# Optimization experiments

Measured on AMD Instinct MI355X. Metric: run time of the kernel, lower is better.

The kernel has to match this reference:

```python
import jax, jax.numpy as jnp
import numpy as np

# ---- dims ----
B0, CIN, Hh, Ww = 8, 256, 96, 96
SPLIT = 8
DM = CIN // SPLIT            # 32  per-split d_model
EXPAND = 2
DIN = EXPAND * DM            # 64  d_inner
DSTATE = 64
DCONV = 3
HEADDIM = 8
NH = DIN // HEADDIM          # 8 heads
DOUT = 256
CHUNK = 32
D_IN_PROJ = 2 * DIN + 2 * DSTATE + NH  # 264
CONV_CH = DIN + 2 * DSTATE   # 192


def setup_inputs() -> dict:
    key = jax.random.key(0)
    ks = jax.random.split(key, 10)
    x = jax.random.normal(ks[0], (B0, CIN, Hh, Ww), jnp.float32)
    inp = {
        'x': x,
        'ln_w': jnp.ones((CIN,), jnp.float32),
        'ln_b': jnp.zeros((CIN,), jnp.float32),
        'skip_scale': jnp.ones((1,), jnp.float32),
        'proj_w': jax.random.normal(ks[1], (CIN, DOUT), jnp.float32) / np.sqrt(CIN),
        'proj_b': jnp.zeros((DOUT,), jnp.float32),
        'W_in': jax.random.normal(ks[2], (DM, D_IN_PROJ), jnp.float32) / np.sqrt(DM),
        'conv_w': jax.random.normal(ks[3], (CONV_CH, 1, DCONV), jnp.float32) * 0.3,
        'conv_b': jnp.zeros((CONV_CH,), jnp.float32),
        'dt_bias': jax.random.normal(ks[4], (NH,), jnp.float32) * 0.5,
        'A_log': jnp.log(jnp.arange(1.0, NH + 1.0, dtype=jnp.float32)),
        'D': jax.random.normal(ks[5], (NH,), jnp.float32) * 0.5,
        'rms_w': jnp.ones((DIN,), jnp.float32),
        'W_out': jax.random.normal(ks[6], (DIN, DM), jnp.float32) / np.sqrt(DIN),
    }
    return inp


def _layernorm(x, w, b, eps=1e-5):
    mu = jnp.mean(x, -1, keepdims=True)
    xc = x - mu
    var = jnp.mean(xc * xc, -1, keepdims=True)
    return xc * jax.lax.rsqrt(var + eps) * w + b


def _ssd(x, A, Bm, Cm, chunk):
    # x: (b,l,h,p)  A: (b,l,h)  Bm/Cm: (b,l,n); chunked SSD (Mamba2 minimal)
    b, l, h, p = x.shape
    n = Bm.shape[-1]
    nc = l // chunk
    xc = x.reshape(b, nc, chunk, h, p)
    Ac = A.reshape(b, nc, chunk, h).transpose(0, 3, 1, 2)  # (b,h,c,l)
    Bc = Bm.reshape(b, nc, chunk, n)
    Cc = Cm.reshape(b, nc, chunk, n)
    ac = jnp.cumsum(Ac, -1)                                 # (b,h,c,l)
    seg = ac[..., :, None] - ac[..., None, :]
    mask = jnp.tril(jnp.ones((chunk, chunk), bool))
    L = jnp.where(mask, jnp.exp(jnp.where(mask, seg, 0.0)), 0.0)  # (b,h,c,l,s)
    Yd = jnp.einsum('bcln,bcsn,bhcls,bcshp->bclhp', Cc, Bc, L, xc)
    decay_states = jnp.exp(ac[..., -1:] - ac)               # (b,h,c,l)
    states = jnp.einsum('bcln,bhcl,bclhp->bchpn', Bc, decay_states, xc)
    chunk_decay = jnp.exp(ac[..., -1])                      # (b,h,c)
    def step(carry, inp):
        s, d = inp
        return carry * d[..., None, None] + s, carry
    states_t = jnp.moveaxis(states, 1, 0)                   # (c,b,h,p,n)
    dec_t = jnp.moveaxis(chunk_decay, 2, 0)                 # (c,b,h)
    _, prev = jax.lax.scan(step, jnp.zeros_like(states_t[0]), (states_t, dec_t))
    prev = jnp.moveaxis(prev, 0, 1)                         # (b,c,h,p,n)
    Yo = jnp.einsum('bcln,bchpn,bhcl->bclhp', Cc, prev, jnp.exp(ac))
    return (Yd + Yo).reshape(b, l, h, p)


def _mamba2(u, W_in, conv_w, conv_b, dt_bias, A_log, D, rms_w, W_out):
    b, l, _ = u.shape
    zxbcdt = u @ W_in
    z = zxbcdt[..., :DIN]
    xBC = zxbcdt[..., DIN:DIN + CONV_CH]
    dt = jax.nn.softplus(zxbcdt[..., -NH:] + dt_bias)       # (b,l,h)
    conv = jax.lax.conv_general_dilated(
        xBC.transpose(0, 2, 1), conv_w, (1,), [(DCONV - 1, 0)],
        dimension_numbers=('NCH', 'OIH', 'NCH'), feature_group_count=CONV_CH)
    xBC = jax.nn.silu(conv + conv_b[None, :, None]).transpose(0, 2, 1)
    xs = xBC[..., :DIN].reshape(b, l, NH, HEADDIM)
    Bm = xBC[..., DIN:DIN + DSTATE]
    Cm = xBC[..., DIN + DSTATE:]
    A = -jnp.exp(A_log)
    y = _ssd(xs * dt[..., None], dt * A, Bm, Cm, CHUNK)
    y = y + xs * D[None, None, :, None]
    y = y.reshape(b, l, DIN) * jax.nn.silu(z)               # gated
    y = y * jax.lax.rsqrt(jnp.mean(y * y, -1, keepdims=True) + 1e-5) * rms_w
    return y @ W_out


def reference(x, ln_w, ln_b, skip_scale, proj_w, proj_b, W_in, conv_w, conv_b,
              dt_bias, A_log, D, rms_w, W_out):
    Bn, C, h, w = x.shape
    L = h * w
    xf = x.reshape(Bn, C, L).transpose(0, 2, 1)             # (B,L,C)
    xn = _layernorm(xf, ln_w, ln_b)
    d = C // SPLIT
    xs = jnp.moveaxis(xn.reshape(Bn, L, SPLIT, d), 2, 0)    # (S,B,L,d)
    xs = xs.reshape(SPLIT * Bn, L, d)
    ym = _mamba2(xs, W_in, conv_w, conv_b, dt_bias, A_log, D, rms_w, W_out)
    ym = ym + skip_scale * xs
    ym = jnp.moveaxis(ym.reshape(SPLIT, Bn, L, d), 0, 2).reshape(Bn, L, C)
    ym = _layernorm(ym, ln_w, ln_b)
    out = ym @ proj_w + proj_b                              # (B,L,DOUT)
    return out.transpose(0, 2, 1).reshape(Bn, DOUT, h, w)
```

## Files before the change

### kernel.cpp

```cpp
#include <hip/hip_runtime.h>
#include <hip/hip_fp16.h>
#include <math.h>

typedef unsigned short u16;
typedef unsigned int u32;
typedef _Float16 half2_t __attribute__((ext_vector_type(2)));
typedef _Float16 f16x8 __attribute__((ext_vector_type(8)));
typedef float f32x4 __attribute__((ext_vector_type(4)));

#define B0N 8
#define LSEQ 9216
#define NSEQ 64
#define NCHUNK 288
#define DM 32
#define DPROJ 264
#define CONVCH 192
#define XC4 208
#define URH 40
#define CHH 204
#define ZBS 66
#define CH2S 129
#define TTS 40
#define GS 36
#define YH5 264

#ifndef __has_builtin
#define __has_builtin(x) 0
#endif

__device__ __forceinline__ float silu_(float v) { return v / (1.f + __expf(-v)); }

__global__ __launch_bounds__(256) void k1_ln_split(const float* __restrict__ x,
                                                   const float* __restrict__ lnw,
                                                   const float* __restrict__ lnb,
                                                   __half* __restrict__ u) {
  __shared__ float tile[256 * 33];
  __shared__ float mu[32], rs[32], wv[256], bv[256];
  __shared__ float ps[32 * 9], ps2[32 * 9];
  const int b = blockIdx.y, l0 = blockIdx.x * 32, t = threadIdx.x;
  wv[t] = lnw[t];
  bv[t] = lnb[t];
#pragma unroll 4
  for (int i = 0; i < 32; ++i) {
    int c = i * 8 + (t >> 5), ll = t & 31;
    tile[c * 33 + ll] = x[((size_t)b * 256 + c) * LSEQ + l0 + ll];
  }
  __syncthreads();
  {
    const int ll = t & 31, seg = t >> 5;
    float s = 0.f, s2 = 0.f;
#pragma unroll 8
    for (int i = 0; i < 32; ++i) {
      float v = tile[(seg * 32 + i) * 33 + ll];
      s += v; s2 += v * v;
    }
    ps[ll * 9 + seg] = s;
    ps2[ll * 9 + seg] = s2;
  }
  __syncthreads();
  if (t < 32) {
    float s = 0.f, s2 = 0.f;
#pragma unroll
    for (int seg = 0; seg < 8; ++seg) { s += ps[t * 9 + seg]; s2 += ps2[t * 9 + seg]; }
    float m = s * (1.f / 256.f);
    mu[t] = m;
    rs[t] = rsqrtf(s2 * (1.f / 256.f) - m * m + 1e-5f);
  }
  __syncthreads();
#pragma unroll 4
  for (int i = 0; i < 32; ++i) {
    int sp = i >> 2, sub = i & 3;
    int ll = sub * 8 + (t >> 5), dm = t & 31;
    int c = sp * 32 + dm;
    float v = (tile[c * 33 + ll] - mu[ll]) * rs[ll] * wv[c] + bv[c];
    u[(((size_t)(sp * B0N + b)) * LSEQ + l0 + ll) * DM + dm] = __float2half(v);
  }
}

__global__ __launch_bounds__(256, 2) void k2_states(
    const __half* __restrict__ u, const float* __restrict__ Win,
    const float* __restrict__ convw, const float* __restrict__ convb,
    const float* __restrict__ dtbias, const float* __restrict__ Alog,
    __half* __restrict__ S, float* __restrict__ cdec) {
  __shared__ __align__(16) _Float16 ur_h[48 * URH];
  __shared__ __align__(16) float CH2[34 * CH2S];
  __shared__ __align__(16) _Float16 xst[64 * TTS];
  __shared__ __align__(16) _Float16 Bt[64 * TTS];
  __shared__ __align__(16) float dtraw[256], dtv[256], acs[256], wv2[256];
  const int c = blockIdx.x, sq = blockIdx.y, t = threadIdx.x;
  const int l0 = c * 32;
  const int lane = t & 63, wvi = t >> 6, g = lane >> 4, c16 = lane & 15;
  const size_t ubase = (size_t)sq * (LSEQ * DM);
  const f32x4 zero4 = {0.f, 0.f, 0.f, 0.f};

  for (int idx = t; idx < 48 * 32; idx += 256) {
    int r = idx >> 5, dm = idx & 31;
    int l = l0 - 2 + r;
    _Float16 v = (_Float16)0.f;
    if (r < 34 && l >= 0) v = ((const _Float16*)u)[ubase + (size_t)l * DM + dm];
    ur_h[r * URH + dm] = v;
  }
  f16x8 bfr[2];
#pragma unroll
  for (int i = 0; i < 2; ++i) {
    int col = 64 + (wvi + i * 4) * 16 + c16;
#pragma unroll
    for (int j = 0; j < 8; ++j) bfr[i][j] = (_Float16)Win[(g * 8 + j) * DPROJ + col];
  }
  __syncthreads();

  {
    f16x8 am[3];
#pragma unroll
    for (int mt = 0; mt < 3; ++mt)
      am[mt] = *(const f16x8*)&ur_h[(mt * 16 + c16) * URH + g * 8];
#pragma unroll
    for (int i = 0; i < 2; ++i) {
      int colc = (wvi + i * 4) * 16 + c16;
#pragma unroll
      for (int mt = 0; mt < 3; ++mt) {
        f32x4 acc = __builtin_amdgcn_mfma_f32_16x16x32_f16(am[mt], bfr[i], zero4, 0, 0, 0);
#pragma unroll
        for (int r = 0; r < 4; ++r) {
          int R = mt * 16 + 4 * g + r;
          if (R < 34) CH2[R * CH2S + colc] = acc[r];
        }
      }
    }
  }
  __syncthreads();

  {
    const int ch0 = t & 63, lb = t >> 6;
    float cw[2][3], cb[2];
#pragma unroll
    for (int cr = 0; cr < 2; ++cr) {
      int ch = ch0 + cr * 64;
      cw[cr][0] = convw[ch * 3 + 0];
      cw[cr][1] = convw[ch * 3 + 1];
      cw[cr][2] = convw[ch * 3 + 2];
      cb[cr] = convb[ch];
    }
#pragma unroll
    for (int lr = 0; lr < 8; ++lr) {
      int l = lb + lr * 4;
#pragma unroll
      for (int cr = 0; cr < 2; ++cr) {
        int ch = ch0 + cr * 64;
        float v = CH2[l * CH2S + ch] * cw[cr][0] + CH2[(l + 1) * CH2S + ch] * cw[cr][1] +
                  CH2[(l + 2) * CH2S + ch] * cw[cr][2] + cb[cr];
        _Float16 sv = (_Float16)silu_(v);
        if (cr == 0) xst[ch * TTS + l] = sv;
        else Bt[(ch - 64) * TTS + l] = sv;
      }
    }
    int l = t >> 3, h = t & 7;
    float raw = 0.f;
#pragma unroll
    for (int dm = 0; dm < 32; ++dm)
      raw += (float)ur_h[(l + 2) * URH + dm] * Win[dm * DPROJ + 256 + h];
    dtraw[l * 8 + h] = raw;
  }
  __syncthreads();

  {
    const int l = t & 31, h = t >> 5;
    float raw = dtraw[l * 8 + h] + dtbias[h];
    float dt = (raw > 20.f) ? raw : log1pf(__expf(raw));
    float x = dt;
#pragma unroll
    for (int d = 1; d < 32; d <<= 1) {
      float y = __shfl_up(x, d, 32);
      if (l >= d) x += y;
    }
    const float A = -__expf(Alog[h]);
    dtv[t] = dt;
    acs[t] = A * x;
    if (l == 31) cdec[(sq * NCHUNK + c) * 8 + h] = __expf(A * x);
  }
  __syncthreads();

  _Float16* Ah = (_Float16*)CH2;
  {
    int h = t >> 5;
    wv2[t] = __expf(acs[h * 32 + 31] - acs[t]) * dtv[t];
  }
  __syncthreads();
  {
    const int hp = t >> 2, lb2 = (t & 3) * 8;
    const float* w = &wv2[(hp >> 3) * 32 + lb2];
    const _Float16* xr = &xst[hp * TTS + lb2];
    _Float16* ar = &Ah[hp * TTS + lb2];
#pragma unroll
    for (int i = 0; i < 8; ++i) ar[i] = (_Float16)((float)xr[i] * w[i]);
  }
  __syncthreads();

  __half* Sout = (__half*)((char*)CH2 + 5120);
  {
    const int mt = wvi;
    f16x8 aS = *(const f16x8*)&Ah[(mt * 16 + c16) * TTS + g * 8];
#pragma unroll
    for (int nt = 0; nt < 4; ++nt) {
      f16x8 bS = *(const f16x8*)&Bt[(nt * 16 + c16) * TTS + g * 8];
      f32x4 acc = __builtin_amdgcn_mfma_f32_16x16x32_f16(aS, bS, zero4, 0, 0, 0);
#pragma unroll
      for (int r = 0; r < 4; ++r)
        Sout[(mt * 16 + 4 * g + r) * 72 + nt * 16 + c16] = __float2half(acc[r]);
    }
  }
  __syncthreads();
  const size_t sbase = (size_t)(sq * NCHUNK + c) * 4096;
#pragma unroll
  for (int i = 0; i < 2; ++i) {
    int idx = i * 256 + t;
    int hp = idx >> 3, part = idx & 7;
    *(uint4*)(S + sbase + hp * 64 + part * 8) = *(const uint4*)&Sout[hp * 72 + part * 8];
  }
}

__global__ __launch_bounds__(512) void k3_scan(__half* __restrict__ S,
                                               const float* __restrict__ cdec) {
  const int sq = blockIdx.x >> 3, h = blockIdx.x & 7, t = threadIdx.x;
  float carry = 0.f;
  for (int c = 0; c < NCHUNK; ++c) {
    size_t idx = (size_t)(sq * NCHUNK + c) * 4096 + h * 512 + t;
    float s = __half2float(S[idx]);
    S[idx] = __float2half(carry);
    carry = carry * cdec[(sq * NCHUNK + c) * 8 + h] + s;
  }
}

__global__ __launch_bounds__(256, 4) void k4_out(
    const __half* __restrict__ u, const float* __restrict__ Win,
    const float* __restrict__ convw, const float* __restrict__ convb,
    const float* __restrict__ dtbias, const float* __restrict__ Alog,
    const float* __restrict__ Dp, const float* __restrict__ rmsw,
    const float* __restrict__ Wout, const float* __restrict__ skip,
    const __half* __restrict__ S, __half* __restrict__ ym) {
  __shared__ __align__(16) _Float16 ur_h[48 * URH];
  __shared__ __align__(16) _Float16 CHh[34 * CHH];
  __shared__ __align__(16) __half xch[32 * XC4];
  __shared__ __align__(16) float dtraw[256];
  __shared__ __align__(16) float dtv[256], acs[256];
  __shared__ __align__(16) _Float16 zbuf[32 * ZBS];
  const int c = blockIdx.x, sq = blockIdx.y, t = threadIdx.x;
  const int l0 = c * 32;
  const int lane = t & 63, wvi = t >> 6, g = lane >> 4, c16 = lane & 15;
  const size_t ubase = (size_t)sq * (LSEQ * DM);
  const f32x4 zero4 = {0.f, 0.f, 0.f, 0.f};

  const size_t sbase = (size_t)(sq * NCHUNK + c) * 4096;
  uint4 sv0, sv1;
  {
    const uint4* sp = (const uint4*)(S + sbase);
    sv0 = sp[t * 2];
    sv1 = sp[t * 2 + 1];
  }
  for (int idx = t; idx < 48 * 32; idx += 256) {
    int r = idx >> 5, dm = idx & 31;
    int l = l0 - 2 + r;
    _Float16 v = (_Float16)0.f;
    if (r < 34 && l >= 0) v = ((const _Float16*)u)[ubase + (size_t)l * DM + dm];
    ur_h[r * URH + dm] = v;
  }
  f16x8 bfr[3];
#pragma unroll
  for (int i = 0; i < 3; ++i) {
    int col = 64 + (wvi + i * 4) * 16 + c16;
#pragma unroll
    for (int j = 0; j < 8; ++j) bfr[i][j] = (_Float16)Win[(g * 8 + j) * DPROJ + col];
  }
  f16x8 bz;
  {
    int col = wvi * 16 + c16;
#pragma unroll
    for (int j = 0; j < 8; ++j) bz[j] = (_Float16)Win[(g * 8 + j) * DPROJ + col];
  }
  __syncthreads();

  {
    f16x8 am[3];
#pragma unroll
    for (int mt = 0; mt < 3; ++mt)
      am[mt] = *(const f16x8*)&ur_h[(mt * 16 + c16) * URH + g * 8];
#pragma unroll
    for (int i = 0; i < 3; ++i) {
      int colc = (wvi + i * 4) * 16 + c16;
#pragma unroll
      for (int mt = 0; mt < 3; ++mt) {
        f32x4 acc = __builtin_amdgcn_mfma_f32_16x16x32_f16(am[mt], bfr[i], zero4, 0, 0, 0);
#pragma unroll
        for (int r = 0; r < 4; ++r) {
          int R = mt * 16 + 4 * g + r;
          if (R < 34) CHh[R * CHH + colc] = (_Float16)acc[r];
        }
      }
    }
#pragma unroll
    for (int mz = 0; mz < 2; ++mz) {
      f16x8 az = *(const f16x8*)&ur_h[(2 + mz * 16 + c16) * URH + g * 8];
      f32x4 acc = __builtin_amdgcn_mfma_f32_16x16x32_f16(az, bz, zero4, 0, 0, 0);
#pragma unroll
      for (int r = 0; r < 4; ++r) {
        int lY = mz * 16 + 4 * g + r;
        zbuf[lY * ZBS + wvi * 16 + c16] = (_Float16)acc[r];
      }
    }
  }
  __syncthreads();

  {
    const int ch0 = t & 63, lbq = t >> 6;
#pragma unroll
    for (int cr = 0; cr < 3; ++cr) {
      int ch = ch0 + cr * 64;
      float w0 = convw[ch * 3 + 0], w1 = convw[ch * 3 + 1], w2 = convw[ch * 3 + 2];
      float cb = convb[ch];
      float a = (float)CHh[(lbq * 8 + 0) * CHH + ch];
      float b = (float)CHh[(lbq * 8 + 1) * CHH + ch];
#pragma unroll
      for (int j = 0; j < 8; ++j) {
        float cn = (float)CHh[(lbq * 8 + j + 2) * CHH + ch];
        float v = a * w0 + b * w1 + cn * w2 + cb;
        xch[(lbq * 8 + j) * XC4 + ch] = __float2half(silu_(v));
        a = b; b = cn;
      }
    }
    int l = t >> 3, h = t & 7;
    float raw = 0.f;
#pragma unroll
    for (int dm = 0; dm < 32; ++dm)
      raw += (float)ur_h[(l + 2) * URH + dm] * Win[dm * DPROJ + 256 + h];
    dtraw[l * 8 + h] = raw;
  }
  __syncthreads();

  {
    char* pvb = (char*)CHh;
    int hp = t >> 2, part = t & 3;
    *(uint4*)(pvb + hp * 144 + part * 32) = sv0;
    *(uint4*)(pvb + hp * 144 + part * 32 + 16) = sv1;
  }
  {
    const int l = t & 31, h = t >> 5;
    float raw = dtraw[l * 8 + h] + dtbias[h];
    float dt = (raw > 20.f) ? raw : log1pf(__expf(raw));
    float x = dt;
#pragma unroll
    for (int d = 1; d < 32; d <<= 1) {
      float y = __shfl_up(x, d, 32);
      if (l >= d) x += y;
    }
    dtv[t] = dt;
    acs[t] = -__expf(Alog[h]) * x;
  }
  __syncthreads();

  float* Gm = (float*)((char*)CHh + 9216);
  {
    float ev = __expf(acs[t]);
    dtraw[t] = ev;
    const int mt = wvi >> 1, nt = wvi & 1;
    f32x4 acc = zero4;
#pragma unroll
    for (int kk = 0; kk < 2; ++kk) {
      f16x8 aC = *(const f16x8*)&xch[(mt * 16 + c16) * XC4 + 128 + kk * 32 + g * 8];
      f16x8 bB = *(const f16x8*)&xch[(nt * 16 + c16) * XC4 + 64 + kk * 32 + g * 8];
      acc = __builtin_amdgcn_mfma_f32_16x16x32_f16(aC, bB, acc, 0, 0, 0);
    }
#pragma unroll
    for (int r = 0; r < 4; ++r)
      Gm[(mt * 16 + 4 * g + r) * GS + nt * 16 + c16] = acc[r];
  }
  __syncthreads();

  {
    const int s2b = g * 8;
    float gv[2][8];
#pragma unroll
    for (int mt = 0; mt < 2; ++mt) {
      const float* gr = &Gm[(mt * 16 + c16) * GS + s2b];
      float4 g0 = *(const float4*)gr;
      float4 g1 = *(const float4*)(gr + 4);
      gv[mt][0] = g0.x; gv[mt][1] = g0.y; gv[mt][2] = g0.z; gv[mt][3] = g0.w;
      gv[mt][4] = g1.x; gv[mt][5] = g1.y; gv[mt][6] = g1.z; gv[mt][7] = g1.w;
    }
#pragma unroll
    for (int hh = 0; hh < 2; ++hh) {
      const int h = 2 * wvi + hh;
      const float* ap = &acs[h * 32 + s2b];
      const float* dp = &dtv[h * 32 + s2b];
      float4 a0 = *(const float4*)ap, a1 = *(const float4*)(ap + 4);
      float4 d0 = *(const float4*)dp, d1 = *(const float4*)(dp + 4);
      const float av[8] = {a0.x, a0.y, a0.z, a0.w, a1.x, a1.y, a1.z, a1.w};
      const float dv[8] = {d0.x, d0.y, d0.z, d0.w, d1.x, d1.y, d1.z, d1.w};
      f16x8 bfr2;
#pragma unroll
      for (int j = 0; j < 8; ++j)
        bfr2[j] = *(const _Float16*)&xch[(s2b + j) * XC4 + h * 8 + (c16 & 7)];
#pragma unroll
      for (int mt = 0; mt < 2; ++mt) {
        const int row = mt * 16 + c16;
        const float arow = acs[h * 32 + row];
        f16x8 afr;
#pragma unroll
        for (int j = 0; j < 8; ++j) {
          float m = gv[mt][j] * __expf(arow - av[j]) * dv[j];
          afr[j] = (_Float16)((s2b + j <= row) ? m : 0.f);
        }
        f32x4 dacc = __builtin_amdgcn_mfma_f32_16x16x32_f16(afr, bfr2, zero4, 0, 0, 0);
        if (c16 < 8) {
#pragma unroll
          for (int r = 0; r < 4; ++r)
            xch[(mt * 16 + 4 * g + r) * XC4 + 64 + h * 8 + c16] = __float2half(dacc[r]);
        }
      }
    }
  }
  __syncthreads();

  {
    const __half* pvh = (const __half*)CHh;
#pragma unroll
    for (int mt = 0; mt < 2; ++mt) {
      f32x4 acc = zero4;
#pragma unroll
      for (int kk = 0; kk < 2; ++kk) {
        f16x8 aC = *(const f16x8*)&xch[(mt * 16 + c16) * XC4 + 128 + kk * 32 + g * 8];
        f16x8 bP = *(const f16x8*)&pvh[(wvi * 16 + c16) * 72 + kk * 32 + g * 8];
        acc = __builtin_amdgcn_mfma_f32_16x16x32_f16(aC, bP, acc, 0, 0, 0);
      }
      int hp = wvi * 16 + c16;
#pragma unroll
      for (int r = 0; r < 4; ++r) {
        int l = mt * 16 + 4 * g + r;
        float e = dtraw[(hp >> 3) * 32 + l];
        __half* yb = &xch[l * XC4 + 64 + hp];
        *yb = __float2half(__half2float(*yb) + acc[r] * e);
      }
    }
  }
  __syncthreads();

  {
    const int hp = t & 63;
    const float dcoef = Dp[hp >> 3];
#pragma unroll
    for (int k = 0; k < 8; ++k) {
      int l = (k * 256 + t) >> 6;
      float y = __half2float(xch[l * XC4 + 64 + hp]) + (float)xch[l * XC4 + hp] * dcoef;
      float z = (float)zbuf[l * ZBS + hp];
      y *= z / (1.f + __expf(-z));
      xch[l * XC4 + 64 + hp] = __float2half(y);
    }
  }
  __syncthreads();

  float* rp = Gm;
  float* scl = (float*)ur_h;
  {
    const int l = t & 31, seg = t >> 5;
    float p = 0.f;
#pragma unroll
    for (int k = 0; k < 8; ++k) {
      float v = __half2float(xch[l * XC4 + 64 + seg * 8 + k]);
      p += v * v;
    }
    rp[l * 9 + seg] = p;
  }
  __syncthreads();
  if (t < 32) {
    float s2s = 0.f;
#pragma unroll
    for (int seg = 0; seg < 8; ++seg) s2s += rp[t * 9 + seg];
    scl[t] = rsqrtf(s2s * (1.f / 64.f) + 1e-5f);
  }
  __syncthreads();

  for (int idx = t; idx < 2048; idx += 256) {
    int l = idx >> 6, hp = idx & 63;
    xch[l * XC4 + 64 + hp] =
        __float2half(__half2float(xch[l * XC4 + 64 + hp]) * scl[l] * rmsw[hp]);
  }
  __syncthreads();

  {
    const float skipv = skip[0];
    const int mt = wvi >> 1, nt = wvi & 1;
    f32x4 acc = zero4;
#pragma unroll
    for (int kk = 0; kk < 2; ++kk) {
      f16x8 aY = *(const f16x8*)&xch[(mt * 16 + c16) * XC4 + 64 + kk * 32 + g * 8];
      f16x8 bW;
#pragma unroll
      for (int j = 0; j < 8; ++j)
        bW[j] = (_Float16)Wout[(kk * 32 + g * 8 + j) * 32 + nt * 16 + c16];
      acc = __builtin_amdgcn_mfma_f32_16x16x32_f16(aY, bW, acc, 0, 0, 0);
    }
#pragma unroll
    for (int r = 0; r < 4; ++r) {
      int l = mt * 16 + 4 * g + r;
      int dm = nt * 16 + c16;
      size_t gi = ubase + (size_t)(l0 + l) * DM + dm;
      ym[gi] = __float2half(acc[r] + skipv * __half2float(u[gi]));
    }
  }
}

__global__ __launch_bounds__(256, 4) void k5_ln_proj(const __half* __restrict__ ym,
                                                     const float* __restrict__ lnw,
                                                     const float* __restrict__ lnb,
                                                     const float* __restrict__ pw,
                                                     const float* __restrict__ pb,
                                                     float* __restrict__ outp) {
  __shared__ __align__(16) char buf[33792];
  __shared__ float mu[32], rs[32], wv[256], bv[256];
  __shared__ float ps[32 * 9], ps2[32 * 9];
  _Float16* yh = (_Float16*)buf;
  float* res = (float*)buf;
  const int b = blockIdx.y, l0 = blockIdx.x * 32, t = threadIdx.x;
  const int lane = t & 63, wvi = t >> 6, g = lane >> 4, c16 = lane & 15;
  const f32x4 zero4 = {0.f, 0.f, 0.f, 0.f};
  wv[t] = lnw[t];
  bv[t] = lnb[t];
  for (int sp = 0; sp < 8; ++sp) {
#pragma unroll
    for (int i = 0; i < 2; ++i) {
      int idx = i * 256 + t;
      int ll = idx >> 4, dmp = (idx & 15) * 2;
      u32 v = *(const u32*)&ym[(((size_t)(sp * B0N + b)) * LSEQ + l0 + ll) * DM + dmp];
      *(u32*)&yh[ll * YH5 + sp * 32 + dmp] = v;
    }
  }
  __syncthreads();
  {
    const int ll = t & 31, seg = t >> 5;
    float s = 0.f, s2 = 0.f;
#pragma unroll 8
    for (int i = 0; i < 32; ++i) {
      float v = (float)yh[ll * YH5 + seg * 32 + i];
      s += v; s2 += v * v;
    }
    ps[ll * 9 + seg] = s;
    ps2[ll * 9 + seg] = s2;
  }
  __syncthreads();
  if (t < 32) {
    float s = 0.f, s2 = 0.f;
#pragma unroll
    for (int seg = 0; seg < 8; ++seg) { s += ps[t * 9 + seg]; s2 += ps2[t * 9 + seg]; }
    float m = s * (1.f / 256.f);
    mu[t] = m;
    rs[t] = rsqrtf(s2 * (1.f / 256.f) - m * m + 1e-5f);
  }
  __syncthreads();
#pragma unroll
  for (int i = 0; i < 32; ++i) {
    int idx = i * 256 + t;
    int ll = idx >> 8, ch = idx & 255;
    float v = ((float)yh[ll * YH5 + ch] - mu[ll]) * rs[ll] * wv[ch] + bv[ch];
    yh[ll * YH5 + ch] = (_Float16)v;
  }
  __syncthreads();
  f16x8 am[16];
#pragma unroll
  for (int mt = 0; mt < 2; ++mt)
#pragma unroll
    for (int kk = 0; kk < 8; ++kk)
      am[mt * 8 + kk] = *(const f16x8*)&yh[(mt * 16 + c16) * YH5 + kk * 32 + g * 8];
  __syncthreads();
#pragma unroll
  for (int ni = 0; ni < 4; ++ni) {
    const int col = (wvi + ni * 4) * 16 + c16;
    f32x4 acc0 = zero4, acc1 = zero4;
#pragma unroll
    for (int kk = 0; kk < 8; ++kk) {
      f16x8 bW;
#pragma unroll
      for (int j = 0; j < 8; ++j)
        bW[j] = (_Float16)pw[(size_t)(kk * 32 + g * 8 + j) * 256 + col];
      acc0 = __builtin_amdgcn_mfma_f32_16x16x32_f16(am[kk], bW, acc0, 0, 0, 0);
      acc1 = __builtin_amdgcn_mfma_f32_16x16x32_f16(am[8 + kk], bW, acc1, 0, 0, 0);
    }
    const float bias = pb[col];
#pragma unroll
    for (int r = 0; r < 4; ++r) {
      res[col * 33 + 4 * g + r] = acc0[r] + bias;
      res[col * 33 + 16 + 4 * g + r] = acc1[r] + bias;
    }
  }
  __syncthreads();
  for (int idx = t; idx < 8192; idx += 256) {
    int o = idx >> 5, l = idx & 31;
    outp[((size_t)(b * 256 + o)) * LSEQ + l0 + l] = res[o * 33 + l];
  }
}

extern "C" void kernel_launch(void* const* d_in, const int* in_sizes, int n_in,
                              void* d_out, int out_size, void* d_ws, size_t ws_size,
                              hipStream_t stream) {
  (void)in_sizes; (void)n_in; (void)out_size;
  const float* x     = (const float*)d_in[0];
  const float* lnw   = (const float*)d_in[1];
  const float* lnb   = (const float*)d_in[2];
  const float* skip  = (const float*)d_in[3];
  const float* pw    = (const float*)d_in[4];
  const float* pb    = (const float*)d_in[5];
  const float* Win   = (const float*)d_in[6];
  const float* convw = (const float*)d_in[7];
  const float* convb = (const float*)d_in[8];
  const float* dtb   = (const float*)d_in[9];
  const float* Alog  = (const float*)d_in[10];
  const float* Dp    = (const float*)d_in[11];
  const float* rmsw  = (const float*)d_in[12];
  const float* Wout  = (const float*)d_in[13];
  float* outp = (float*)d_out;

  const size_t NEED = 227082240ull;
  if (ws_size < NEED) return;
  char* ws = (char*)d_ws;
  __half* u    = (__half*)ws;
  __half* S    = (__half*)(ws + 37748736);
  float*  cdec = (float*)(ws + 188743680);
  __half* ym   = (__half*)(ws + 189333504);

  k1_ln_split<<<dim3(288, 8), 256, 0, stream>>>(x, lnw, lnb, u);
  k2_states<<<dim3(288, 64), 256, 0, stream>>>(u, Win, convw, convb, dtb, Alog, S, cdec);
  k3_scan<<<dim3(512), 512, 0, stream>>>(S, cdec);
  k4_out<<<dim3(288, 64), 256, 0, stream>>>(u, Win, convw, convb, dtb, Alog, Dp, rmsw,
                                            Wout, skip, S, ym);
  k5_ln_proj<<<dim3(288, 8), 256, 0, stream>>>(ym, lnw, lnb, pw, pb, outp);
}
```

Baseline: 636.5 us.

## Shrink k2 shared memory with fp16 staging for occupancy; vectorize and prefetch k3 scan

k2_states now stages the in-projection result in fp16 and packs all shared buffers into one aliased byte array. This cuts LDS use enough to raise the launch bound from 2 to 5 blocks per CU. The conv step is rewritten so each thread slides over 8 consecutive positions and writes them as one 8-wide vector store. k3_scan uses 128 threads that each handle 4 contiguous state values, caches the decay factors in shared memory, and prefetches four chunks ahead to hide the serial dependency on global-memory latency. The fp16 intermediate adds a small precision loss.

```diff
diff --git a/kernel.cpp b/kernel.cpp
--- a/kernel.cpp
+++ b/kernel.cpp
@@ -19,7 +19,7 @@
 #define URH 40
 #define CHH 204
 #define ZBS 66
-#define CH2S 129
+#define C2H 132
 #define TTS 40
 #define GS 36
 #define YH5 264
@@ -77,16 +77,22 @@
   }
 }
 
-__global__ __launch_bounds__(256, 2) void k2_states(
+__global__ __launch_bounds__(256, 5) void k2_states(
     const __half* __restrict__ u, const float* __restrict__ Win,
     const float* __restrict__ convw, const float* __restrict__ convb,
     const float* __restrict__ dtbias, const float* __restrict__ Alog,
     __half* __restrict__ S, float* __restrict__ cdec) {
-  __shared__ __align__(16) _Float16 ur_h[48 * URH];
-  __shared__ __align__(16) float CH2[34 * CH2S];
-  __shared__ __align__(16) _Float16 xst[64 * TTS];
-  __shared__ __align__(16) _Float16 Bt[64 * TTS];
-  __shared__ __align__(16) float dtraw[256], dtv[256], acs[256], wv2[256];
+  __shared__ __align__(16) char smem[32512];
+  _Float16* ur_h = (_Float16*)smem;
+  _Float16* CH2h = (_Float16*)(smem + 3840);
+  _Float16* Ah   = (_Float16*)(smem + 3840);
+  __half*   Sout = (__half*)(smem + 8960);
+  _Float16* xst  = (_Float16*)(smem + 18176);
+  _Float16* Bt   = (_Float16*)(smem + 23296);
+  float* dtraw = (float*)(smem + 28416);
+  float* dtv   = (float*)(smem + 29440);
+  float* acs   = (float*)(smem + 30464);
+  float* wv2   = (float*)(smem + 31488);
   const int c = blockIdx.x, sq = blockIdx.y, t = threadIdx.x;
   const int l0 = c * 32;
   const int lane = t & 63, wvi = t >> 6, g = lane >> 4, c16 = lane & 15;
@@ -123,7 +129,7 @@
 #pragma unroll
         for (int r = 0; r < 4; ++r) {
           int R = mt * 16 + 4 * g + r;
-          if (R < 34) CH2[R * CH2S + colc] = acc[r];
+          if (R < 34) CH2h[R * C2H + colc] = (_Float16)acc[r];
         }
       }
     }
@@ -131,28 +137,23 @@
   __syncthreads();
 
   {
-    const int ch0 = t & 63, lb = t >> 6;
-    float cw[2][3], cb[2];
+    const int ch0 = t & 63, lbq = t >> 6;
 #pragma unroll
     for (int cr = 0; cr < 2; ++cr) {
       int ch = ch0 + cr * 64;
-      cw[cr][0] = convw[ch * 3 + 0];
-      cw[cr][1] = convw[ch * 3 + 1];
-      cw[cr][2] = convw[ch * 3 + 2];
-      cb[cr] = convb[ch];
-    }
-#pragma unroll
-    for (int lr = 0; lr < 8; ++lr) {
-      int l = lb + lr * 4;
-#pragma unroll
-      for (int cr = 0; cr < 2; ++cr) {
-        int ch = ch0 + cr * 64;
-        float v = CH2[l * CH2S + ch] * cw[cr][0] + CH2[(l + 1) * CH2S + ch] * cw[cr][1] +
-                  CH2[(l + 2) * CH2S + ch] * cw[cr][2] + cb[cr];
-        _Float16 sv = (_Float16)silu_(v);
-        if (cr == 0) xst[ch * TTS + l] = sv;
-        else Bt[(ch - 64) * TTS + l] = sv;
-      }
+      float w0 = convw[ch * 3 + 0], w1 = convw[ch * 3 + 1], w2 = convw[ch * 3 + 2];
+      float cb = convb[ch];
+      float a = (float)CH2h[(lbq * 8 + 0) * C2H + ch];
+      float b = (float)CH2h[(lbq * 8 + 1) * C2H + ch];
+      f16x8 out;
+#pragma unroll
+      for (int j = 0; j < 8; ++j) {
+        float cn = (float)CH2h[(lbq * 8 + j + 2) * C2H + ch];
+        out[j] = (_Float16)silu_(a * w0 + b * w1 + cn * w2 + cb);
+        a = b; b = cn;
+      }
+      if (cr == 0) *(f16x8*)&xst[ch0 * TTS + lbq * 8] = out;
+      else         *(f16x8*)&Bt[ch0 * TTS + lbq * 8] = out;
     }
     int l = t >> 3, h = t & 7;
     float raw = 0.f;
@@ -180,7 +181,6 @@
   }
   __syncthreads();
 
-  _Float16* Ah = (_Float16*)CH2;
   {
     int h = t >> 5;
     wv2[t] = __expf(acs[h * 32 + 31] - acs[t]) * dtv[t];
@@ -190,13 +190,13 @@
     const int hp = t >> 2, lb2 = (t & 3) * 8;
     const float* w = &wv2[(hp >> 3) * 32 + lb2];
     const _Float16* xr = &xst[hp * TTS + lb2];
-    _Float16* ar = &Ah[hp * TTS + lb2];
-#pragma unroll
-    for (int i = 0; i < 8; ++i) ar[i] = (_Float16)((float)xr[i] * w[i]);
-  }
-  __syncthreads();
-
-  __half* Sout = (__half*)((char*)CH2 + 5120);
+    f16x8 ov;
+#pragma unroll
+    for (int i = 0; i < 8; ++i) ov[i] = (_Float16)((float)xr[i] * w[i]);
+    *(f16x8*)&Ah[hp * TTS + lb2] = ov;
+  }
+  __syncthreads();
+
   {
     const int mt = wvi;
     f16x8 aS = *(const f16x8*)&Ah[(mt * 16 + c16) * TTS + g * 8];
@@ -219,15 +219,39 @@
   }
 }
 
-__global__ __launch_bounds__(512) void k3_scan(__half* __restrict__ S,
+__global__ __launch_bounds__(128) void k3_scan(__half* __restrict__ S,
                                                const float* __restrict__ cdec) {
+  __shared__ float cd[NCHUNK];
   const int sq = blockIdx.x >> 3, h = blockIdx.x & 7, t = threadIdx.x;
-  float carry = 0.f;
-  for (int c = 0; c < NCHUNK; ++c) {
-    size_t idx = (size_t)(sq * NCHUNK + c) * 4096 + h * 512 + t;
-    float s = __half2float(S[idx]);
-    S[idx] = __float2half(carry);
-    carry = carry * cdec[(sq * NCHUNK + c) * 8 + h] + s;
+  for (int i = t; i < NCHUNK; i += 128) cd[i] = cdec[(sq * NCHUNK + i) * 8 + h];
+  __syncthreads();
+  __half* p = S + (size_t)sq * NCHUNK * 4096 + h * 512 + t * 4;
+  uint2 f0 = *(const uint2*)(p);
+  uint2 f1 = *(const uint2*)(p + 4096);
+  uint2 f2 = *(const uint2*)(p + 2 * 4096);
+  uint2 f3 = *(const uint2*)(p + 3 * 4096);
+  float car0 = 0.f, car1 = 0.f, car2 = 0.f, car3 = 0.f;
+  for (int c = 0; c < NCHUNK; c += 4) {
+#define K3_STEP(F, K)                                                              \
+    {                                                                              \
+      half2_t lo = *(half2_t*)&F.x, hi = *(half2_t*)&F.y;                          \
+      float s0 = (float)lo.x, s1 = (float)lo.y, s2 = (float)hi.x, s3 = (float)hi.y;\
+      int nc = c + K + 4; if (nc > NCHUNK - 1) nc = NCHUNK - 1;                    \
+      F = *(const uint2*)(p + (size_t)nc * 4096);                                  \
+      half2_t olo, ohi;                                                            \
+      olo.x = (_Float16)car0; olo.y = (_Float16)car1;                              \
+      ohi.x = (_Float16)car2; ohi.y = (_Float16)car3;                              \
+      uint2 ov; ov.x = *(u32*)&olo; ov.y = *(u32*)&ohi;                            \
+      *(uint2*)(p + (size_t)(c + K) * 4096) = ov;                                  \
+      float d = cd[c + K];                                                         \
+      car0 = car0 * d + s0; car1 = car1 * d + s1;                                  \
+      car2 = car2 * d + s2; car3 = car3 * d + s3;                                  \
+    }
+    K3_STEP(f0, 0)
+    K3_STEP(f1, 1)
+    K3_STEP(f2, 2)
+    K3_STEP(f3, 3)
+#undef K3_STEP
   }
 }
 
@@ -627,7 +651,7 @@
 
   k1_ln_split<<<dim3(288, 8), 256, 0, stream>>>(x, lnw, lnb, u);
   k2_states<<<dim3(288, 64), 256, 0, stream>>>(u, Win, convw, convb, dtb, Alog, S, cdec);
-  k3_scan<<<dim3(512), 512, 0, stream>>>(S, cdec);
+  k3_scan<<<dim3(512), 128, 0, stream>>>(S, cdec);
   k4_out<<<dim3(288, 64), 256, 0, stream>>>(u, Win, convw, convb, dtb, Alog, Dp, rmsw,
                                             Wout, skip, S, ym);
   k5_ln_proj<<<dim3(288, 8), 256, 0, stream>>>(ym, lnw, lnb, pw, pb, outp);
```

Result: no change. 638.3 us (+0.3%).
